# Kernel optimization log

Measured on AMD Instinct MI355X. Metric: run time of the kernel, lower is better.

Reference implementation:

```python
import jax, jax.numpy as jnp
import numpy as np

IMG, P, C = 512, 16, 1
D, DEPTH, H, DH, MLP = 768, 12, 8, 64, 2048
GRID = IMG // P          # 32
NP = GRID * GRID         # 1024 patches
N = NP + 1               # +cls token
EPS = 1e-5


def _ln(x, s, b):
    m = jnp.mean(x, -1, keepdims=True)
    v = jnp.mean((x - m) ** 2, -1, keepdims=True)
    return (x - m) * jax.lax.rsqrt(v + EPS) * s + b


def setup_inputs() -> dict:
    key = jax.random.key(0)
    ks = jax.random.split(key, 12)
    s = 0.02
    f32 = jnp.float32
    return {
        "x": jax.random.normal(ks[0], (4, C, IMG, IMG), f32),
        "conv_w": jax.random.normal(ks[1], (D, C, P, P), f32) * s,   # [out,in,kh,kw] like torch
        "conv_b": jnp.zeros((D,), f32),
        "cls_token": jax.random.normal(ks[2], (1, 1, D), f32),
        "pos_emb": jax.random.normal(ks[3], (1, N, D), f32),
        "qkv_w": jax.random.normal(ks[4], (DEPTH, D, 3 * H * DH), f32) * s,  # [in,out] layout
        "merge_w": jax.random.normal(ks[5], (DEPTH, H * DH, D), f32) * s,
        "merge_b": jnp.zeros((DEPTH, D), f32),
        "ln1_s": jnp.ones((DEPTH, D), f32),
        "ln1_b": jnp.zeros((DEPTH, D), f32),
        "ln2_s": jnp.ones((DEPTH, D), f32),
        "ln2_b": jnp.zeros((DEPTH, D), f32),
        "ffn_w1": jax.random.normal(ks[6], (DEPTH, D, MLP), f32) * s,
        "ffn_b1": jnp.zeros((DEPTH, MLP), f32),
        "ffn_w2": jax.random.normal(ks[7], (DEPTH, MLP, D), f32) * s,
        "ffn_b2": jnp.zeros((DEPTH, D), f32),
        "lnf_s": jnp.ones((D,), f32),
        "lnf_b": jnp.zeros((D,), f32),
    }


def reference(x, conv_w, conv_b, cls_token, pos_emb, qkv_w, merge_w, merge_b,
              ln1_s, ln1_b, ln2_s, ln2_b, ffn_w1, ffn_b1, ffn_w2, ffn_b2,
              lnf_s, lnf_b):
    B = x.shape[0]
    # Patch embed: stride-P conv == non-overlapping patch extraction + matmul
    xr = x.reshape(B, C, GRID, P, GRID, P)
    tok = jnp.einsum('bchpwq,dcpq->bhwd', xr, conv_w).reshape(B, NP, D) + conv_b
    t = jnp.concatenate([jnp.broadcast_to(cls_token, (B, 1, D)), tok], axis=1)
    t = t + pos_emb  # dropout is identity in eval
    scale = DH ** -0.5
    for i in range(DEPTH):
        # MSA with pre-LN
        h = _ln(t, ln1_s[i], ln1_b[i])
        qkv = (h @ qkv_w[i]).reshape(B, N, H, 3, DH)   # [B,N,H,3,DH]
        q = jnp.transpose(qkv[..., 0, :], (0, 2, 1, 3))  # [B,H,N,DH]
        k = jnp.transpose(qkv[..., 1, :], (0, 2, 1, 3))
        v = jnp.transpose(qkv[..., 2, :], (0, 2, 1, 3))
        att = jax.nn.softmax(jnp.einsum('bhnd,bhmd->bhnm', q, k) * scale, axis=-1)
        o = jnp.einsum('bhnm,bhmd->bhnd', att, v)
        o = jnp.transpose(o, (0, 2, 1, 3)).reshape(B, N, H * DH)
        t = t + (o @ merge_w[i] + merge_b[i])
        # FFN with pre-LN, exact (erf) GELU like torch nn.GELU
        h2 = _ln(t, ln2_s[i], ln2_b[i])
        f = jax.nn.gelu(h2 @ ffn_w1[i] + ffn_b1[i], approximate=False)
        t = t + (f @ ffn_w2[i] + ffn_b2[i])
    return _ln(t, lnf_s, lnf_b)
```

## Files before the change

kernel.cpp:

```cpp
#include <hip/hip_runtime.h>

#define DEV __device__ __forceinline__

typedef short s8v __attribute__((ext_vector_type(8)));
typedef float f4v __attribute__((ext_vector_type(4)));

DEV short f2bf(float f) {
  unsigned u = __float_as_uint(f);
  u += 0x7FFFu + ((u >> 16) & 1u);
  return (short)(u >> 16);
}
DEV float bf2f(short s) { return __uint_as_float(((unsigned)(unsigned short)s) << 16); }

DEV void gld_lds16(const short* g, short* l) {
  __builtin_amdgcn_global_load_lds(
      (const __attribute__((address_space(1))) void*)g,
      (__attribute__((address_space(3))) void*)l, 16, 0, 0);
}

DEV int xcd_swz(int id, int nwg) {
  int q8 = nwg >> 3, r8 = nwg & 7, xcd = id & 7, off = id >> 3;
  return (xcd < r8) ? (xcd * (q8 + 1) + off) : (r8 * (q8 + 1) + (xcd - r8) * q8 + off);
}

__global__ __launch_bounds__(256) void gemm64(
    const short* __restrict__ A, const short* __restrict__ B, void* __restrict__ Cv,
    const float* __restrict__ bias,
    int M, int N, int K, int lda, int ldb, int ldc, int flags)
{
  __shared__ __align__(16) short As[2][64 * 64];
  __shared__ __align__(16) short Bs[2][128 * 64];
  int nwg = gridDim.x * gridDim.y;
  int idl = blockIdx.y * gridDim.x + blockIdx.x;
  int swz = xcd_swz(idl, nwg);
  int bx = swz % gridDim.x, by = swz / gridDim.x;
  int m0 = by * 64, n0 = bx * 128;
  int tid = threadIdx.x, lane = tid & 63, w = tid >> 6;
  int lr = lane & 15, kg = lane >> 4;
  f4v acc[4][2] = {};
  int NT = K >> 6;

#define STAGE(bufi, k0)                                                   \
  {                                                                       \
    _Pragma("unroll")                                                     \
    for (int p = 0; p < 2; ++p) {                                         \
      int ch = p * 256 + w * 64 + lane;                                   \
      int row = ch >> 3, c = (ch & 7) ^ (row & 7);                        \
      gld_lds16(A + (long)(m0 + row) * lda + (k0) + c * 8,                \
                &As[bufi][(p * 256 + w * 64) * 8]);                       \
    }                                                                     \
    _Pragma("unroll")                                                     \
    for (int p = 0; p < 4; ++p) {                                         \
      int ch = p * 256 + w * 64 + lane;                                   \
      int row = ch >> 3, c = (ch & 7) ^ (row & 7);                        \
      gld_lds16(B + (long)(n0 + row) * ldb + (k0) + c * 8,                \
                &Bs[bufi][(p * 256 + w * 64) * 8]);                       \
    }                                                                     \
  }

  STAGE(0, 0)
  for (int t = 0; t < NT; ++t) {
    int buf = t & 1;
    if (t + 1 < NT) {
      STAGE(buf ^ 1, (t + 1) * 64)
      asm volatile("s_waitcnt vmcnt(6)" ::: "memory");
    } else {
      asm volatile("s_waitcnt vmcnt(0)" ::: "memory");
    }
    __builtin_amdgcn_s_barrier();
    #pragma unroll
    for (int ks = 0; ks < 2; ++ks) {
      s8v av[4], bv[2];
      #pragma unroll
      for (int mi = 0; mi < 4; ++mi) {
        int row = mi * 16 + lr;
        int sl = (ks * 4 + kg) ^ (row & 7);
        av[mi] = *(const s8v*)&As[buf][row * 64 + sl * 8];
      }
      #pragma unroll
      for (int ni = 0; ni < 2; ++ni) {
        int row = w * 32 + ni * 16 + lr;
        int sl = (ks * 4 + kg) ^ (row & 7);
        bv[ni] = *(const s8v*)&Bs[buf][row * 64 + sl * 8];
      }
      #pragma unroll
      for (int mi = 0; mi < 4; ++mi)
        #pragma unroll
        for (int ni = 0; ni < 2; ++ni)
          acc[mi][ni] = __builtin_amdgcn_mfma_f32_16x16x32_bf16(av[mi], bv[ni], acc[mi][ni], 0, 0, 0);
    }
    asm volatile("s_waitcnt lgkmcnt(0)" ::: "memory");
    __builtin_amdgcn_s_barrier();
  }
#undef STAGE

  float* Cf = (float*)Cv;
  short* Cb = (short*)Cv;
  #pragma unroll
  for (int mi = 0; mi < 4; ++mi)
    #pragma unroll
    for (int ni = 0; ni < 2; ++ni) {
      int col = n0 + w * 32 + ni * 16 + lr;
      float bvv = (flags & 1) ? bias[col] : 0.f;
      #pragma unroll
      for (int j = 0; j < 4; ++j) {
        int row = m0 + mi * 16 + kg * 4 + j;
        if (row >= M) continue;
        float v = acc[mi][ni][j] + bvv;
        if (flags & 2) v = 0.5f * v * (1.f + erff(v * 0.70710678118f));
        long ci = (long)row * ldc + col;
        if (flags & 8) Cb[ci] = f2bf(v);
        else { if (flags & 4) v += Cf[ci]; Cf[ci] = v; }
      }
    }
}

__global__ __launch_bounds__(256) void flash_k(
    const short* __restrict__ qkv, short* __restrict__ O)
{
  int swz = xcd_swz(blockIdx.x, 544);
  int z = swz / 17, qt = swz - z * 17;
  int zb = z >> 3, zh = z & 7;
  const short* base = qkv + (long)zb * 1025 * 1536 + zh * 192;
  const short* Qg = base;
  const short* Kg = base + 64;
  const short* Vg = base + 128;
  int q0 = qt * 64;
  int tid = threadIdx.x, lane = tid & 63, w = tid >> 6;
  int lr = lane & 15, kg = lane >> 4;

  __shared__ __align__(16) short Qs[64][72];
  __shared__ __align__(16) short Ks[2][64 * 64];
  __shared__ __align__(16) short Vt[2][64][72];
  __shared__ __align__(16) short Ps[4][16][72];

  for (int s = tid; s < 512; s += 256) {
    int row = s >> 3, ch = s & 7;
    s8v v = {};
    if (q0 + row < 1025) v = *(const s8v*)(Qg + (long)(q0 + row) * 1536 + ch * 8);
    *(s8v*)&Qs[row][ch * 8] = v;
  }
  __syncthreads();
  s8v aq[2];
  aq[0] = *(const s8v*)&Qs[w * 16 + lr][kg * 8];
  aq[1] = *(const s8v*)&Qs[w * 16 + lr][32 + kg * 8];

#define STAGE_K(bufi, kv0)                                                 \
  {                                                                        \
    int s0 = w * 128;                                                      \
    _Pragma("unroll")                                                      \
    for (int i = 0; i < 2; ++i) {                                          \
      int s = s0 + i * 64 + lane;                                          \
      int row = s >> 3, c = (s & 7) ^ (row & 7);                           \
      gld_lds16(Kg + (long)((kv0) + row) * 1536 + c * 8,                   \
                &Ks[bufi][(s0 + i * 64) * 8]);                             \
    }                                                                      \
  }

  f4v acc[4] = {};
  float m_run[4], l_run[4];
  #pragma unroll
  for (int j = 0; j < 4; ++j) { m_run[j] = -3.0e38f; l_run[j] = 0.f; }

  STAGE_K(0, 0)
  {
    #pragma unroll
    for (int p = 0; p < 2; ++p) {
      int s = p * 256 + tid;
      int key = s & 63, ch = s >> 6;
      s8v v = {};
      if (key < 1025) v = *(const s8v*)(Vg + (long)key * 1536 + ch * 8);
      #pragma unroll
      for (int j = 0; j < 8; ++j) Vt[0][ch * 8 + j][key] = v[j];
    }
  }
  asm volatile("s_waitcnt vmcnt(0)" ::: "memory");
  asm volatile("s_waitcnt lgkmcnt(0)" ::: "memory");
  __builtin_amdgcn_s_barrier();

  for (int kt = 0; kt < 17; ++kt) {
    int cur = kt & 1;
    int kv0 = kt * 64;
    s8v vreg[2];
    int vok[2];
    if (kt < 16) {
      STAGE_K(cur ^ 1, kv0 + 64)
      #pragma unroll
      for (int p = 0; p < 2; ++p) {
        int s = p * 256 + tid;
        int key = (s & 63) + kv0 + 64, ch = s >> 6;
        vok[p] = key < 1025;
        vreg[p] = vok[p] ? *(const s8v*)(Vg + (long)key * 1536 + ch * 8) : s8v{};
      }
    }

    f4v sa[4] = {};
    #pragma unroll
    for (int ni = 0; ni < 4; ++ni) {
      int row = ni * 16 + lr;
      #pragma unroll
      for (int ks = 0; ks < 2; ++ks) {
        int c = (ks * 4 + kg) ^ (row & 7);
        s8v bk = *(const s8v*)&Ks[cur][row * 64 + c * 8];
        sa[ni] = __builtin_amdgcn_mfma_f32_16x16x32_bf16(aq[ks], bk, sa[ni], 0, 0, 0);
      }
    }
    float sv[4][4], pv[4][4], tm[4], ts[4];
    #pragma unroll
    for (int j = 0; j < 4; ++j) tm[j] = -3.0e38f;
    #pragma unroll
    for (int ni = 0; ni < 4; ++ni) {
      bool valid = (kv0 + ni * 16 + lr) < 1025;
      #pragma unroll
      for (int j = 0; j < 4; ++j) {
        float s = valid ? sa[ni][j] * 0.125f : -3.0e38f;
        sv[ni][j] = s;
        tm[j] = fmaxf(tm[j], s);
      }
    }
    #pragma unroll
    for (int o = 1; o < 16; o <<= 1)
      #pragma unroll
      for (int j = 0; j < 4; ++j) tm[j] = fmaxf(tm[j], __shfl_xor(tm[j], o));
    float scale[4], m_new[4];
    #pragma unroll
    for (int j = 0; j < 4; ++j) {
      m_new[j] = fmaxf(m_run[j], tm[j]);
      scale[j] = __expf(m_run[j] - m_new[j]);
      m_run[j] = m_new[j];
      ts[j] = 0.f;
    }
    #pragma unroll
    for (int ni = 0; ni < 4; ++ni)
      #pragma unroll
      for (int j = 0; j < 4; ++j) {
        float p = __expf(sv[ni][j] - m_new[j]);
        pv[ni][j] = p;
        ts[j] += p;
      }
    #pragma unroll
    for (int o = 1; o < 16; o <<= 1)
      #pragma unroll
      for (int j = 0; j < 4; ++j) ts[j] += __shfl_xor(ts[j], o);
    #pragma unroll
    for (int j = 0; j < 4; ++j) l_run[j] = l_run[j] * scale[j] + ts[j];
    #pragma unroll
    for (int ni = 0; ni < 4; ++ni)
      #pragma unroll
      for (int j = 0; j < 4; ++j) acc[ni][j] *= scale[j];

    if (kt < 16) {
      #pragma unroll
      for (int p = 0; p < 2; ++p) {
        int s = p * 256 + tid;
        int key = s & 63, ch = s >> 6;
        s8v v = vok[p] ? vreg[p] : s8v{};
        #pragma unroll
        for (int j = 0; j < 8; ++j) Vt[cur ^ 1][ch * 8 + j][key] = v[j];
      }
    }

    #pragma unroll
    for (int ni = 0; ni < 4; ++ni)
      #pragma unroll
      for (int j = 0; j < 4; ++j)
        Ps[w][kg * 4 + j][ni * 16 + lr] = f2bf(pv[ni][j]);
    asm volatile("s_waitcnt lgkmcnt(0)" ::: "memory");
    s8v ap[2];
    ap[0] = *(const s8v*)&Ps[w][lr][kg * 8];
    ap[1] = *(const s8v*)&Ps[w][lr][32 + kg * 8];
    #pragma unroll
    for (int ni = 0; ni < 4; ++ni) {
      #pragma unroll
      for (int ks = 0; ks < 2; ++ks) {
        s8v bvv = *(const s8v*)&Vt[cur][ni * 16 + lr][ks * 32 + kg * 8];
        acc[ni] = __builtin_amdgcn_mfma_f32_16x16x32_bf16(ap[ks], bvv, acc[ni], 0, 0, 0);
      }
    }
    asm volatile("s_waitcnt lgkmcnt(0)" ::: "memory");
    asm volatile("s_waitcnt vmcnt(0)" ::: "memory");
    __builtin_amdgcn_s_barrier();
  }
#undef STAGE_K

  float inv[4];
  #pragma unroll
  for (int j = 0; j < 4; ++j) inv[j] = 1.f / l_run[j];
  #pragma unroll
  for (int ni = 0; ni < 4; ++ni)
    #pragma unroll
    for (int j = 0; j < 4; ++j) {
      int row = q0 + w * 16 + kg * 4 + j;
      if (row < 1025)
        O[((long)(zb * 1025 + row)) * 512 + zh * 64 + ni * 16 + lr] = f2bf(acc[ni][j] * inv[j]);
    }
}

DEV void tconv_body(const float* w, short* wt, int K, int N, int bx, int by, int tid)
{
  __shared__ float tile[32][33];
  int n0 = bx * 32, k0 = by * 32;
  int tx = tid & 31, ty = tid >> 5;
  #pragma unroll
  for (int j = 0; j < 4; ++j)
    tile[ty + j * 8][tx] = w[(long)(k0 + ty + j * 8) * N + n0 + tx];
  __syncthreads();
  #pragma unroll
  for (int j = 0; j < 4; ++j)
    wt[(long)(n0 + ty + j * 8) * K + k0 + tx] = f2bf(tile[tx][ty + j * 8]);
}

__global__ __launch_bounds__(256) void tconv4_k(
    const float* __restrict__ sq, const float* __restrict__ sm,
    const float* __restrict__ sf1, const float* __restrict__ sf2,
    short* __restrict__ dq, short* __restrict__ dm,
    short* __restrict__ df1, short* __restrict__ df2)
{
  int id = blockIdx.x, tid = threadIdx.x;
  if (id < 1152)       tconv_body(sq,  dq,  768, 1536, id % 48,          id / 48,          tid);
  else if (id < 1536)  tconv_body(sm,  dm,  512, 768,  (id - 1152) % 24, (id - 1152) / 24, tid);
  else if (id < 3072)  tconv_body(sf1, df1, 768, 2048, (id - 1536) % 64, (id - 1536) / 64, tid);
  else                 tconv_body(sf2, df2, 2048, 768, (id - 3072) % 24, (id - 3072) / 24, tid);
}

__global__ __launch_bounds__(256) void cvt_k(const float* __restrict__ in,
    short* __restrict__ out, int n)
{
  int i = blockIdx.x * 256 + threadIdx.x;
  if (i < n) out[i] = f2bf(in[i]);
}

DEV void st_ln(float* p, float v) { *p = v; }
DEV void st_ln(short* p, float v) { *p = f2bf(v); }

template<typename OT>
__global__ __launch_bounds__(256) void ln_k(const float* __restrict__ x,
    const float* __restrict__ g, const float* __restrict__ b,
    OT* __restrict__ y, int rows)
{
  int row = blockIdx.x;
  if (row >= rows) return;
  const float* xr = x + (long)row * 768;
  OT* yr = y + (long)row * 768;
  int t = threadIdx.x;
  float v0 = xr[t], v1 = xr[t + 256], v2 = xr[t + 512];
  float s = v0 + v1 + v2, s2 = v0 * v0 + v1 * v1 + v2 * v2;
  #pragma unroll
  for (int o = 32; o > 0; o >>= 1) { s += __shfl_down(s, o); s2 += __shfl_down(s2, o); }
  __shared__ float as_[4], as2_[4];
  if ((t & 63) == 0) { as_[t >> 6] = s; as2_[t >> 6] = s2; }
  __syncthreads();
  s = as_[0] + as_[1] + as_[2] + as_[3];
  s2 = as2_[0] + as2_[1] + as2_[2] + as2_[3];
  float mean = s * (1.f / 768.f);
  float var = s2 * (1.f / 768.f) - mean * mean;
  float r = rsqrtf(var + 1e-5f);
  st_ln(&yr[t],       (v0 - mean) * r * g[t]       + b[t]);
  st_ln(&yr[t + 256], (v1 - mean) * r * g[t + 256] + b[t + 256]);
  st_ln(&yr[t + 512], (v2 - mean) * r * g[t + 512] + b[t + 512]);
}

__global__ __launch_bounds__(256) void im2col_k(const float* __restrict__ x,
    short* __restrict__ A)
{
  int i = blockIdx.x * 256 + threadIdx.x;
  int k = i & 255, row = i >> 8;
  int px = k & 15, py = k >> 4;
  int gx = row & 31, gy = (row >> 5) & 31, b = row >> 10;
  A[i] = f2bf(x[((long)(b * 512) + gy * 16 + py) * 512 + gx * 16 + px]);
}

__global__ __launch_bounds__(256) void assemble_k(const short* __restrict__ tok,
    const float* __restrict__ cls, const float* __restrict__ pos, float* __restrict__ t)
{
  int i = blockIdx.x * 256 + threadIdx.x;
  int d = i % 768; int rn = i / 768; int n = rn % 1025; int b = rn / 1025;
  float v = (n == 0) ? cls[d] : bf2f(tok[((long)(b * 1024 + n - 1)) * 768 + d]);
  t[i] = v + pos[n * 768 + d];
}

extern "C" void kernel_launch(void* const* d_in, const int* in_sizes, int n_in,
                              void* d_out, int out_size, void* d_ws, size_t ws_size,
                              hipStream_t stream)
{
  const float* x       = (const float*)d_in[0];
  const float* conv_w  = (const float*)d_in[1];
  const float* conv_b  = (const float*)d_in[2];
  const float* cls     = (const float*)d_in[3];
  const float* pos     = (const float*)d_in[4];
  const float* qkv_w   = (const float*)d_in[5];
  const float* merge_w = (const float*)d_in[6];
  const float* merge_b = (const float*)d_in[7];
  const float* ln1_s   = (const float*)d_in[8];
  const float* ln1_b   = (const float*)d_in[9];
  const float* ln2_s   = (const float*)d_in[10];
  const float* ln2_b   = (const float*)d_in[11];
  const float* ffn_w1  = (const float*)d_in[12];
  const float* ffn_b1  = (const float*)d_in[13];
  const float* ffn_w2  = (const float*)d_in[14];
  const float* ffn_b2  = (const float*)d_in[15];
  const float* lnf_s   = (const float*)d_in[16];
  const float* lnf_b   = (const float*)d_in[17];

  char* wsp = (char*)d_ws;
  size_t o = 0;
  auto take = [&](size_t bytes) { char* r = wsp + o; o = (o + bytes + 255) & ~(size_t)255; return r; };
  short* wq   = (short*)take(1536ul * 768 * 2);
  short* wm   = (short*)take(768ul * 512 * 2);
  short* wf1  = (short*)take(2048ul * 768 * 2);
  short* wf2  = (short*)take(768ul * 2048 * 2);
  short* wcv  = (short*)take(768ul * 256 * 2);
  float* t    = (float*)take(4100ul * 768 * 4);
  char*  hO   = take(4352ul * 768 * 2);
  short* qkv  = (short*)take(4ul * 1025 * 1536 * 2);
  char*  fV   = take(4352ul * 2048 * 2);
  take(2ul << 20);

  short* h   = (short*)hO;
  short* O   = (short*)hO;
  short* f   = (short*)fV;
  short* imc = (short*)fV;
  short* tok = (short*)(fV + 4096ul * 256 * 2);

  dim3 blk(256);

  cvt_k<<<768, blk, 0, stream>>>(conv_w, wcv, 768 * 256);
  im2col_k<<<4096, blk, 0, stream>>>(x, imc);
  gemm64<<<dim3(6, 64), blk, 0, stream>>>(imc, wcv, tok, conv_b,
      4096, 768, 256, 256, 256, 768, 1 | 8);
  assemble_k<<<12300, blk, 0, stream>>>(tok, cls, pos, t);

  for (int i = 0; i < 12; ++i) {
    tconv4_k<<<4608, blk, 0, stream>>>(
        qkv_w + (long)i * 768 * 1536, merge_w + (long)i * 512 * 768,
        ffn_w1 + (long)i * 768 * 2048, ffn_w2 + (long)i * 2048 * 768,
        wq, wm, wf1, wf2);

    ln_k<short><<<4100, blk, 0, stream>>>(t, ln1_s + i * 768, ln1_b + i * 768, h, 4100);
    gemm64<<<dim3(12, 65), blk, 0, stream>>>(h, wq, qkv, nullptr,
        4100, 1536, 768, 768, 768, 1536, 8);
    flash_k<<<544, blk, 0, stream>>>(qkv, O);
    gemm64<<<dim3(6, 65), blk, 0, stream>>>(O, wm, t, merge_b + i * 768,
        4100, 768, 512, 512, 512, 768, 1 | 4);
    ln_k<short><<<4100, blk, 0, stream>>>(t, ln2_s + i * 768, ln2_b + i * 768, h, 4100);
    gemm64<<<dim3(16, 65), blk, 0, stream>>>(h, wf1, f, ffn_b1 + i * 2048,
        4100, 2048, 768, 768, 768, 2048, 1 | 2 | 8);
    gemm64<<<dim3(6, 65), blk, 0, stream>>>(f, wf2, t, ffn_b2 + i * 768,
        4100, 768, 2048, 2048, 2048, 768, 1 | 4);
  }
  ln_k<float><<<4100, blk, 0, stream>>>(t, lnf_s, lnf_b, (float*)d_out, 4100);
}
```

Measured before the change: 2.452 ms.

## Add per-shape GEMM tilings and trim flash attention LDS and rounding cost

Adds a 128x128-tile GEMM for the wide QKV and FFN1 projections and a 64x64-tile template for the narrow N=768 GEMMs, so that tile reuse and grid occupancy suit each shape. The narrow GEMMs double their block count to fill more CUs, and the wide ones cut redundant A/B loads per output. Flash attention reuses the Q LDS buffer for P, drops the bounds check on the first V tile, switches to a cheaper round-half-up bf16 conversion, and raises wave priority around the MFMA blocks. The new rounding differs slightly from round-to-nearest-even, and the 128-row tiles load A rows past M=4100 for the last tile (the buffers appear padded to 4352 rows).

```diff
diff --git a/kernel.cpp b/kernel.cpp
--- a/kernel.cpp
+++ b/kernel.cpp
@@ -10,6 +10,9 @@
   u += 0x7FFFu + ((u >> 16) & 1u);
   return (short)(u >> 16);
 }
+DEV short f2bf_fast(float f) {
+  return (short)((__float_as_uint(f) + 0x8000u) >> 16);
+}
 DEV float bf2f(short s) { return __uint_as_float(((unsigned)(unsigned short)s) << 16); }
 
 DEV void gld_lds16(const short* g, short* l) {
@@ -23,21 +26,26 @@
   return (xcd < r8) ? (xcd * (q8 + 1) + off) : (r8 * (q8 + 1) + (xcd - r8) * q8 + off);
 }
 
-__global__ __launch_bounds__(256) void gemm64(
+template<int BN>
+__global__ __launch_bounds__(256) void gemm_t(
     const short* __restrict__ A, const short* __restrict__ B, void* __restrict__ Cv,
     const float* __restrict__ bias,
     int M, int N, int K, int lda, int ldb, int ldc, int flags)
 {
+  constexpr int BPASS = BN / 32;
+  constexpr int MI = (BN == 128) ? 4 : 2;
   __shared__ __align__(16) short As[2][64 * 64];
-  __shared__ __align__(16) short Bs[2][128 * 64];
+  __shared__ __align__(16) short Bs[2][BN * 64];
   int nwg = gridDim.x * gridDim.y;
   int idl = blockIdx.y * gridDim.x + blockIdx.x;
   int swz = xcd_swz(idl, nwg);
   int bx = swz % gridDim.x, by = swz / gridDim.x;
-  int m0 = by * 64, n0 = bx * 128;
+  int m0 = by * 64, n0 = bx * BN;
   int tid = threadIdx.x, lane = tid & 63, w = tid >> 6;
   int lr = lane & 15, kg = lane >> 4;
-  f4v acc[4][2] = {};
+  int wrb = (BN == 128) ? 0 : (w >> 1) * 32;
+  int wcb = (BN == 128) ? w * 32 : (w & 1) * 32;
+  f4v acc[MI][2] = {};
   int NT = K >> 6;
 
 #define STAGE(bufi, k0)                                                   \
@@ -50,7 +58,7 @@
                 &As[bufi][(p * 256 + w * 64) * 8]);                       \
     }                                                                     \
     _Pragma("unroll")                                                     \
-    for (int p = 0; p < 4; ++p) {                                         \
+    for (int p = 0; p < BPASS; ++p) {                                     \
       int ch = p * 256 + w * 64 + lane;                                   \
       int row = ch >> 3, c = (ch & 7) ^ (row & 7);                        \
       gld_lds16(B + (long)(n0 + row) * ldb + (k0) + c * 8,                \
@@ -63,28 +71,31 @@
     int buf = t & 1;
     if (t + 1 < NT) {
       STAGE(buf ^ 1, (t + 1) * 64)
-      asm volatile("s_waitcnt vmcnt(6)" ::: "memory");
+      if constexpr (BN == 128)
+        asm volatile("s_waitcnt vmcnt(6)" ::: "memory");
+      else
+        asm volatile("s_waitcnt vmcnt(4)" ::: "memory");
     } else {
       asm volatile("s_waitcnt vmcnt(0)" ::: "memory");
     }
     __builtin_amdgcn_s_barrier();
     #pragma unroll
     for (int ks = 0; ks < 2; ++ks) {
-      s8v av[4], bv[2];
-      #pragma unroll
-      for (int mi = 0; mi < 4; ++mi) {
-        int row = mi * 16 + lr;
+      s8v av[MI], bv[2];
+      #pragma unroll
+      for (int mi = 0; mi < MI; ++mi) {
+        int row = wrb + mi * 16 + lr;
         int sl = (ks * 4 + kg) ^ (row & 7);
         av[mi] = *(const s8v*)&As[buf][row * 64 + sl * 8];
       }
       #pragma unroll
       for (int ni = 0; ni < 2; ++ni) {
-        int row = w * 32 + ni * 16 + lr;
+        int row = wcb + ni * 16 + lr;
         int sl = (ks * 4 + kg) ^ (row & 7);
         bv[ni] = *(const s8v*)&Bs[buf][row * 64 + sl * 8];
       }
       #pragma unroll
-      for (int mi = 0; mi < 4; ++mi)
+      for (int mi = 0; mi < MI; ++mi)
         #pragma unroll
         for (int ni = 0; ni < 2; ++ni)
           acc[mi][ni] = __builtin_amdgcn_mfma_f32_16x16x32_bf16(av[mi], bv[ni], acc[mi][ni], 0, 0, 0);
@@ -97,14 +108,102 @@
   float* Cf = (float*)Cv;
   short* Cb = (short*)Cv;
   #pragma unroll
+  for (int mi = 0; mi < MI; ++mi)
+    #pragma unroll
+    for (int ni = 0; ni < 2; ++ni) {
+      int col = n0 + wcb + ni * 16 + lr;
+      float bvv = (flags & 1) ? bias[col] : 0.f;
+      #pragma unroll
+      for (int j = 0; j < 4; ++j) {
+        int row = m0 + wrb + mi * 16 + kg * 4 + j;
+        if (row >= M) continue;
+        float v = acc[mi][ni][j] + bvv;
+        if (flags & 2) v = 0.5f * v * (1.f + erff(v * 0.70710678118f));
+        long ci = (long)row * ldc + col;
+        if (flags & 8) Cb[ci] = f2bf(v);
+        else { if (flags & 4) v += Cf[ci]; Cf[ci] = v; }
+      }
+    }
+}
+
+__global__ __launch_bounds__(256) void gemm128(
+    const short* __restrict__ A, const short* __restrict__ B, void* __restrict__ Cv,
+    const float* __restrict__ bias,
+    int M, int N, int K, int lda, int ldb, int ldc, int flags)
+{
+  __shared__ __align__(16) short As[2][128 * 64];
+  __shared__ __align__(16) short Bs[2][128 * 64];
+  int nwg = gridDim.x * gridDim.y;
+  int idl = blockIdx.y * gridDim.x + blockIdx.x;
+  int swz = xcd_swz(idl, nwg);
+  int bx = swz % gridDim.x, by = swz / gridDim.x;
+  int m0 = by * 128, n0 = bx * 128;
+  int tid = threadIdx.x, lane = tid & 63, w = tid >> 6;
+  int lr = lane & 15, kg = lane >> 4;
+  int wrb = (w >> 1) * 64, wcb = (w & 1) * 64;
+  f4v acc[4][4] = {};
+  int NT = K >> 6;
+
+#define STAGE(bufi, k0)                                                   \
+  {                                                                       \
+    _Pragma("unroll")                                                     \
+    for (int p = 0; p < 4; ++p) {                                         \
+      int ch = p * 256 + w * 64 + lane;                                   \
+      int row = ch >> 3, c = (ch & 7) ^ (row & 7);                        \
+      gld_lds16(A + (long)(m0 + row) * lda + (k0) + c * 8,                \
+                &As[bufi][(p * 256 + w * 64) * 8]);                       \
+      gld_lds16(B + (long)(n0 + row) * ldb + (k0) + c * 8,                \
+                &Bs[bufi][(p * 256 + w * 64) * 8]);                       \
+    }                                                                     \
+  }
+
+  STAGE(0, 0)
+  for (int t = 0; t < NT; ++t) {
+    int buf = t & 1;
+    if (t + 1 < NT) {
+      STAGE(buf ^ 1, (t + 1) * 64)
+      asm volatile("s_waitcnt vmcnt(8)" ::: "memory");
+    } else {
+      asm volatile("s_waitcnt vmcnt(0)" ::: "memory");
+    }
+    __builtin_amdgcn_s_barrier();
+    #pragma unroll
+    for (int ks = 0; ks < 2; ++ks) {
+      s8v av[4], bv[4];
+      #pragma unroll
+      for (int mi = 0; mi < 4; ++mi) {
+        int row = wrb + mi * 16 + lr;
+        int sl = (ks * 4 + kg) ^ (row & 7);
+        av[mi] = *(const s8v*)&As[buf][row * 64 + sl * 8];
+      }
+      #pragma unroll
+      for (int ni = 0; ni < 4; ++ni) {
+        int row = wcb + ni * 16 + lr;
+        int sl = (ks * 4 + kg) ^ (row & 7);
+        bv[ni] = *(const s8v*)&Bs[buf][row * 64 + sl * 8];
+      }
+      #pragma unroll
+      for (int mi = 0; mi < 4; ++mi)
+        #pragma unroll
+        for (int ni = 0; ni < 4; ++ni)
+          acc[mi][ni] = __builtin_amdgcn_mfma_f32_16x16x32_bf16(av[mi], bv[ni], acc[mi][ni], 0, 0, 0);
+    }
+    asm volatile("s_waitcnt lgkmcnt(0)" ::: "memory");
+    __builtin_amdgcn_s_barrier();
+  }
+#undef STAGE
+
+  float* Cf = (float*)Cv;
+  short* Cb = (short*)Cv;
+  #pragma unroll
   for (int mi = 0; mi < 4; ++mi)
     #pragma unroll
-    for (int ni = 0; ni < 2; ++ni) {
-      int col = n0 + w * 32 + ni * 16 + lr;
+    for (int ni = 0; ni < 4; ++ni) {
+      int col = n0 + wcb + ni * 16 + lr;
       float bvv = (flags & 1) ? bias[col] : 0.f;
       #pragma unroll
       for (int j = 0; j < 4; ++j) {
-        int row = m0 + mi * 16 + kg * 4 + j;
+        int row = m0 + wrb + mi * 16 + kg * 4 + j;
         if (row >= M) continue;
         float v = acc[mi][ni][j] + bvv;
         if (flags & 2) v = 0.5f * v * (1.f + erff(v * 0.70710678118f));
@@ -129,21 +228,20 @@
   int tid = threadIdx.x, lane = tid & 63, w = tid >> 6;
   int lr = lane & 15, kg = lane >> 4;
 
-  __shared__ __align__(16) short Qs[64][72];
+  __shared__ __align__(16) short QPs[64][72];
   __shared__ __align__(16) short Ks[2][64 * 64];
   __shared__ __align__(16) short Vt[2][64][72];
-  __shared__ __align__(16) short Ps[4][16][72];
 
   for (int s = tid; s < 512; s += 256) {
     int row = s >> 3, ch = s & 7;
     s8v v = {};
     if (q0 + row < 1025) v = *(const s8v*)(Qg + (long)(q0 + row) * 1536 + ch * 8);
-    *(s8v*)&Qs[row][ch * 8] = v;
+    *(s8v*)&QPs[row][ch * 8] = v;
   }
   __syncthreads();
   s8v aq[2];
-  aq[0] = *(const s8v*)&Qs[w * 16 + lr][kg * 8];
-  aq[1] = *(const s8v*)&Qs[w * 16 + lr][32 + kg * 8];
+  aq[0] = *(const s8v*)&QPs[w * 16 + lr][kg * 8];
+  aq[1] = *(const s8v*)&QPs[w * 16 + lr][32 + kg * 8];
 
 #define STAGE_K(bufi, kv0)                                                 \
   {                                                                        \
@@ -163,16 +261,13 @@
   for (int j = 0; j < 4; ++j) { m_run[j] = -3.0e38f; l_run[j] = 0.f; }
 
   STAGE_K(0, 0)
-  {
-    #pragma unroll
-    for (int p = 0; p < 2; ++p) {
-      int s = p * 256 + tid;
-      int key = s & 63, ch = s >> 6;
-      s8v v = {};
-      if (key < 1025) v = *(const s8v*)(Vg + (long)key * 1536 + ch * 8);
-      #pragma unroll
-      for (int j = 0; j < 8; ++j) Vt[0][ch * 8 + j][key] = v[j];
-    }
+  #pragma unroll
+  for (int p = 0; p < 2; ++p) {
+    int s = p * 256 + tid;
+    int key = s & 63, ch = s >> 6;
+    s8v v = *(const s8v*)(Vg + (long)key * 1536 + ch * 8);
+    #pragma unroll
+    for (int j = 0; j < 8; ++j) Vt[0][ch * 8 + j][key] = v[j];
   }
   asm volatile("s_waitcnt vmcnt(0)" ::: "memory");
   asm volatile("s_waitcnt lgkmcnt(0)" ::: "memory");
@@ -195,6 +290,7 @@
     }
 
     f4v sa[4] = {};
+    __builtin_amdgcn_s_setprio(1);
     #pragma unroll
     for (int ni = 0; ni < 4; ++ni) {
       int row = ni * 16 + lr;
@@ -205,6 +301,7 @@
         sa[ni] = __builtin_amdgcn_mfma_f32_16x16x32_bf16(aq[ks], bk, sa[ni], 0, 0, 0);
       }
     }
+    __builtin_amdgcn_s_setprio(0);
     float sv[4][4], pv[4][4], tm[4], ts[4];
     #pragma unroll
     for (int j = 0; j < 4; ++j) tm[j] = -3.0e38f;
@@ -264,11 +361,12 @@
     for (int ni = 0; ni < 4; ++ni)
       #pragma unroll
       for (int j = 0; j < 4; ++j)
-        Ps[w][kg * 4 + j][ni * 16 + lr] = f2bf(pv[ni][j]);
+        QPs[w * 16 + kg * 4 + j][ni * 16 + lr] = f2bf_fast(pv[ni][j]);
     asm volatile("s_waitcnt lgkmcnt(0)" ::: "memory");
     s8v ap[2];
-    ap[0] = *(const s8v*)&Ps[w][lr][kg * 8];
-    ap[1] = *(const s8v*)&Ps[w][lr][32 + kg * 8];
+    ap[0] = *(const s8v*)&QPs[w * 16 + lr][kg * 8];
+    ap[1] = *(const s8v*)&QPs[w * 16 + lr][32 + kg * 8];
+    __builtin_amdgcn_s_setprio(1);
     #pragma unroll
     for (int ni = 0; ni < 4; ++ni) {
       #pragma unroll
@@ -277,6 +375,7 @@
         acc[ni] = __builtin_amdgcn_mfma_f32_16x16x32_bf16(ap[ks], bvv, acc[ni], 0, 0, 0);
       }
     }
+    __builtin_amdgcn_s_setprio(0);
     asm volatile("s_waitcnt lgkmcnt(0)" ::: "memory");
     asm volatile("s_waitcnt vmcnt(0)" ::: "memory");
     __builtin_amdgcn_s_barrier();
@@ -426,7 +525,7 @@
 
   cvt_k<<<768, blk, 0, stream>>>(conv_w, wcv, 768 * 256);
   im2col_k<<<4096, blk, 0, stream>>>(x, imc);
-  gemm64<<<dim3(6, 64), blk, 0, stream>>>(imc, wcv, tok, conv_b,
+  gemm_t<64><<<dim3(12, 64), blk, 0, stream>>>(imc, wcv, tok, conv_b,
       4096, 768, 256, 256, 256, 768, 1 | 8);
   assemble_k<<<12300, blk, 0, stream>>>(tok, cls, pos, t);
 
@@ -437,15 +536,15 @@
         wq, wm, wf1, wf2);
 
     ln_k<short><<<4100, blk, 0, stream>>>(t, ln1_s + i * 768, ln1_b + i * 768, h, 4100);
-    gemm64<<<dim3(12, 65), blk, 0, stream>>>(h, wq, qkv, nullptr,
+    gemm128<<<dim3(12, 33), blk, 0, stream>>>(h, wq, qkv, nullptr,
         4100, 1536, 768, 768, 768, 1536, 8);
     flash_k<<<544, blk, 0, stream>>>(qkv, O);
-    gemm64<<<dim3(6, 65), blk, 0, stream>>>(O, wm, t, merge_b + i * 768,
+    gemm_t<64><<<dim3(12, 65), blk, 0, stream>>>(O, wm, t, merge_b + i * 768,
         4100, 768, 512, 512, 512, 768, 1 | 4);
     ln_k<short><<<4100, blk, 0, stream>>>(t, ln2_s + i * 768, ln2_b + i * 768, h, 4100);
-    gemm64<<<dim3(16, 65), blk, 0, stream>>>(h, wf1, f, ffn_b1 + i * 2048,
+    gemm128<<<dim3(16, 33), blk, 0, stream>>>(h, wf1, f, ffn_b1 + i * 2048,
         4100, 2048, 768, 768, 768, 2048, 1 | 2 | 8);
-    gemm64<<<dim3(6, 65), blk, 0, stream>>>(f, wf2, t, ffn_b2 + i * 768,
+    gemm_t<64><<<dim3(12, 65), blk, 0, stream>>>(f, wf2, t, ffn_b2 + i * 768,
         4100, 768, 2048, 2048, 2048, 768, 1 | 4);
   }
   ln_k<float><<<4100, blk, 0, stream>>>(t, lnf_s, lnf_b, (float*)d_out, 4100);
```

Result: no change. 2.443 ms (-0.4%).
